# Performance work log

Measured on AMD Instinct MI355X. Metric: run time of the kernel, lower is better.

Reference implementation:

```python
import jax, jax.numpy as jnp
import numpy as np

B, C_CLS, D_WORD, J = 1024, 80, 300, 8000
IMG_CH = 2048

def setup_inputs() -> dict:
    key = jax.random.key(0)
    ks = jax.random.split(key, 9)
    return {
        'feature': jax.random.normal(ks[0], (B, IMG_CH), jnp.float32),
        'inp': jax.random.normal(ks[1], (1, C_CLS, D_WORD), jnp.float32),
        'A': jax.random.uniform(ks[2], (C_CLS, C_CLS), jnp.float32),
        'W_gc1': jax.random.normal(ks[3], (D_WORD, 1024), jnp.float32) * (1.0 / np.sqrt(1024)),
        'W_gc2': jax.random.normal(ks[4], (1024, 2048), jnp.float32) * (1.0 / np.sqrt(2048)),
        'W_img': jax.random.normal(ks[5], (J, IMG_CH), jnp.float32) * 0.02,
        'b_img': jax.random.normal(ks[6], (J,), jnp.float32) * 0.02,
        'W_cls': jax.random.normal(ks[7], (J, 2048), jnp.float32) * 0.02,
        'b_cls': jax.random.normal(ks[8], (J,), jnp.float32) * 0.02,
    }

def _gen_adj(A):
    # torch: D = A.sum(1)**-0.5; adj = (A @ diag(D)).T @ diag(D) = D[:,None]*A.T*D[None,:]
    D = jnp.power(jnp.sum(A, axis=1), -0.5)
    return D[:, None] * A.T * D[None, :]

def reference(feature, inp, A, W_gc1, W_gc2, W_img, b_img, W_cls, b_cls):
    inp0 = inp[0]                                   # [C, 300]
    adj = jax.lax.stop_gradient(_gen_adj(A))        # [C, C], .detach() in torch
    x = adj @ (inp0 @ W_gc1)                        # gc1: [C, 1024]
    x = jax.nn.leaky_relu(x, negative_slope=0.2)
    x = adj @ (x @ W_gc2)                           # gc2: [C, 2048]
    # MFB bilinear pooling (is_usemfb=True, is_hash=False -> out_in_tmp=1, eval-mode dropout=identity)
    # original: out[b,c] = sum_j (Linear_img(feature[b])[j] * Linear_cls(x_col_c)[j])
    img_proj = feature @ W_img.T + b_img            # [B, J]
    cls_proj = x @ W_cls.T + b_cls                  # [C, J]
    x_out = img_proj @ cls_proj.T                   # [B, C]
    return x_out
```

## Files before the change

### kernel.cpp

```cpp
#include <hip/hip_runtime.h>
#include <hip/hip_bf16.h>


typedef __bf16 bf16_t;
typedef __bf16 bf16x8 __attribute__((ext_vector_type(8)));
typedef float f32x4 __attribute__((ext_vector_type(4)));

#define MFMA16(a, b, c) __builtin_amdgcn_mfma_f32_16x16x32_bf16((a), (b), (c), 0, 0, 0)

#define GLOAD_LDS16(g, l)                                     \
  __builtin_amdgcn_global_load_lds(                           \
      (const __attribute__((address_space(1))) void*)(g),     \
      (__attribute__((address_space(3))) void*)(l), 16, 0, 0)

#define PIN()                                   \
  do {                                          \
    asm volatile("" ::: "memory");              \
    __builtin_amdgcn_sched_barrier(0);          \
  } while (0)

__device__ inline bf16x8 cvt8(float4 a, float4 b) {
  bf16x8 v;
  v[0] = (bf16_t)a.x; v[1] = (bf16_t)a.y; v[2] = (bf16_t)a.z; v[3] = (bf16_t)a.w;
  v[4] = (bf16_t)b.x; v[5] = (bf16_t)b.y; v[6] = (bf16_t)b.z; v[7] = (bf16_t)b.w;
  return v;
}

__global__ void k_adj(const float* __restrict__ A, float* __restrict__ adj) {
  __shared__ float Dv[80];
  int tid = threadIdx.x;
  if (tid < 80) {
    float s = 0.f;
    #pragma unroll 4
    for (int j = 0; j < 80; ++j) s += A[tid * 80 + j];
    Dv[tid] = rsqrtf(s);
  }
  __syncthreads();
  for (int idx = tid; idx < 6400; idx += blockDim.x) {
    int i = idx / 80, j = idx % 80;
    adj[idx] = Dv[i] * Dv[j] * A[j * 80 + i];
  }
}

__global__ void k_cvt0(const float* __restrict__ inp0, bf16_t* __restrict__ x0b) {
  int idx = blockIdx.x * blockDim.x + threadIdx.x;
  if (idx < 30720) {
    int c = idx / 384, k = idx % 384;
    x0b[idx] = (k < 300) ? (bf16_t)inp0[c * 300 + k] : (bf16_t)0.f;
  }
}

__global__ __launch_bounds__(256, 2) void k_gc1m(
    const bf16_t* __restrict__ x0b, const float* __restrict__ Wgc1,
    float* __restrict__ t1) {
  int tid = threadIdx.x;
  int w = tid >> 6, l = tid & 63;
  int ln = l & 15, q = l >> 4;
  int n0 = (blockIdx.x & 63) * 16;
  int kc = blockIdx.x >> 6;
  int kq = kc * 128 + w * 32 + q * 8;

  __shared__ float red[4][80][16];
  f32x4 acc[5] = {};
  bf16x8 bfrag;
  #pragma unroll
  for (int jj = 0; jj < 8; ++jj) {
    int k = kq + jj;
    int kcl = k < 300 ? k : 299;
    float wv = Wgc1[kcl * 1024 + n0 + ln];
    bfrag[jj] = (bf16_t)(k < 300 ? wv : 0.f);
  }
  #pragma unroll
  for (int mt = 0; mt < 5; ++mt) {
    bf16x8 afrag = *(const bf16x8*)(x0b + (size_t)(mt * 16 + ln) * 384 + kq);
    acc[mt] = MFMA16(afrag, bfrag, acc[mt]);
  }
  #pragma unroll
  for (int mt = 0; mt < 5; ++mt)
    #pragma unroll
    for (int reg = 0; reg < 4; ++reg)
      red[w][mt * 16 + q * 4 + reg][ln] = acc[mt][reg];
  __syncthreads();
  for (int o = tid; o < 1280; o += 256) {
    int c = o >> 4, nn = o & 15;
    atomicAdd(&t1[c * 1024 + n0 + nn],
              red[0][c][nn] + red[1][c][nn] + red[2][c][nn] + red[3][c][nn]);
  }
}

__global__ void k_adjmul_leaky(const float* __restrict__ adj, const float* __restrict__ t1,
                               bf16_t* __restrict__ x1b) {
  int idx = blockIdx.x * blockDim.x + threadIdx.x;
  int c = idx >> 10, n = idx & 1023;
  const float* ar = adj + c * 80;
  float acc = 0.f;
  #pragma unroll 4
  for (int cc = 0; cc < 80; ++cc) acc += ar[cc] * t1[cc * 1024 + n];
  x1b[idx] = (bf16_t)(acc > 0.f ? acc : 0.2f * acc);
}

__global__ __launch_bounds__(256, 2) void k_gc2m(
    const bf16_t* __restrict__ x1b, const float* __restrict__ Wgc2,
    float* __restrict__ t2) {
  int tid = threadIdx.x;
  int w = tid >> 6, l = tid & 63;
  int ln = l & 15, q = l >> 4;
  int nc = blockIdx.x & 31, kc = blockIdx.x >> 5;

  __shared__ float BsF[2 * 2048];
  auto stage = [&](int b, int k0) {
    #pragma unroll
    for (int it = 0; it < 2; ++it) {
      int slot = tid + it * 256;
      int kr = slot >> 4, nq = slot & 15;
      const float* src = Wgc2 + (size_t)(k0 + kr) * 2048 + nc * 64 + nq * 4;
      float* dst = BsF + b * 2048 + slot * 4;
      GLOAD_LDS16(src, dst);
    }
  };

  int kb = kc * 64;
  bf16x8 a0[5], a1[5];
  #pragma unroll
  for (int mt = 0; mt < 5; ++mt)
    a0[mt] = *(const bf16x8*)(x1b + (size_t)(mt * 16 + ln) * 1024 + kb + q * 8);
  PIN();
  stage(0, kb);
  PIN();
  stage(1, kb + 32);
  PIN();
  #pragma unroll
  for (int mt = 0; mt < 5; ++mt)
    a1[mt] = *(const bf16x8*)(x1b + (size_t)(mt * 16 + ln) * 1024 + kb + 32 + q * 8);
  PIN();

  f32x4 acc[5] = {};
  asm volatile("s_waitcnt vmcnt(7)" ::: "memory");
  PIN();
  __builtin_amdgcn_s_barrier();
  PIN();
  {
    bf16x8 bfrag;
    #pragma unroll
    for (int jj = 0; jj < 8; ++jj) bfrag[jj] = (bf16_t)BsF[(q * 8 + jj) * 64 + w * 16 + ln];
    #pragma unroll
    for (int mt = 0; mt < 5; ++mt) acc[mt] = MFMA16(a0[mt], bfrag, acc[mt]);
  }
  asm volatile("s_waitcnt vmcnt(5)" ::: "memory");
  PIN();
  __builtin_amdgcn_s_barrier();
  PIN();
  {
    bf16x8 bfrag;
    #pragma unroll
    for (int jj = 0; jj < 8; ++jj)
      bfrag[jj] = (bf16_t)BsF[2048 + (q * 8 + jj) * 64 + w * 16 + ln];
    #pragma unroll
    for (int mt = 0; mt < 5; ++mt) acc[mt] = MFMA16(a1[mt], bfrag, acc[mt]);
  }

  #pragma unroll
  for (int mt = 0; mt < 5; ++mt)
    #pragma unroll
    for (int reg = 0; reg < 4; ++reg)
      atomicAdd(&t2[(size_t)(mt * 16 + q * 4 + reg) * 2048 + nc * 64 + w * 16 + ln],
                acc[mt][reg]);
}

__global__ void k_adjmul_bf16(const float* __restrict__ adj, const float* __restrict__ t2,
                              bf16_t* __restrict__ x2) {
  int idx = blockIdx.x * blockDim.x + threadIdx.x;
  int c = idx >> 11, n = idx & 2047;
  const float* ar = adj + c * 80;
  float acc = 0.f;
  #pragma unroll 4
  for (int cc = 0; cc < 80; ++cc) acc += ar[cc] * t2[cc * 2048 + n];
  x2[idx] = (bf16_t)acc;
}

__global__ __launch_bounds__(256, 2) void k_clsproj(
    const float* __restrict__ Wcls, const float* __restrict__ bcls,
    const float* __restrict__ bimg, const bf16_t* __restrict__ x2,
    bf16_t* __restrict__ P, float* __restrict__ r) {
  int tid = threadIdx.x;
  int w = tid >> 6, l = tid & 63;
  int ln = l & 15, q = l >> 4;
  int j0 = blockIdx.x * 16;
  size_t jrow = (size_t)(j0 + ln) * 2048;

  __shared__ float red[4][80][16];
  __shared__ float rloc[80];
  if (tid < 80) rloc[tid] = 0.f;

  f32x4 acc[5] = {};
  int kbase = w * 512 + q * 8;

  float4 bA[2], bB[2];
  bf16x8 aF[2][5];
  {
    const float4* bp = (const float4*)(Wcls + jrow + kbase);
    bA[0] = bp[0]; bB[0] = bp[1];
    #pragma unroll
    for (int mt = 0; mt < 5; ++mt)
      aF[0][mt] = *(const bf16x8*)(x2 + (size_t)(mt * 16 + ln) * 2048 + kbase);
  }
  #pragma unroll
  for (int ks = 0; ks < 16; ++ks) {
    int cur = ks & 1, nxt = cur ^ 1;
    if (ks < 15) {
      int kq = kbase + (ks + 1) * 32;
      const float4* bp = (const float4*)(Wcls + jrow + kq);
      bA[nxt] = bp[0]; bB[nxt] = bp[1];
      #pragma unroll
      for (int mt = 0; mt < 5; ++mt)
        aF[nxt][mt] = *(const bf16x8*)(x2 + (size_t)(mt * 16 + ln) * 2048 + kq);
    }
    bf16x8 bfrag = cvt8(bA[cur], bB[cur]);
    #pragma unroll
    for (int mt = 0; mt < 5; ++mt) acc[mt] = MFMA16(aF[cur][mt], bfrag, acc[mt]);
  }
  #pragma unroll
  for (int mt = 0; mt < 5; ++mt)
    #pragma unroll
    for (int reg = 0; reg < 4; ++reg)
      red[w][mt * 16 + q * 4 + reg][ln] = acc[mt][reg];
  __syncthreads();

  for (int o = tid; o < 1280; o += 256) {
    int c = o >> 4, jj = o & 15;
    float v = red[0][c][jj] + red[1][c][jj] + red[2][c][jj] + red[3][c][jj] + bcls[j0 + jj];
    P[(size_t)c * 8000 + j0 + jj] = (bf16_t)v;
    atomicAdd(&rloc[c], bimg[j0 + jj] * v);
  }
  __syncthreads();
  if (tid < 80) atomicAdd(&r[tid], rloc[tid]);
}

__global__ __launch_bounds__(256, 2) void k_hmat(
    const float* __restrict__ Wimg, const bf16_t* __restrict__ P, float* __restrict__ H) {
  int tid = threadIdx.x;
  int w = tid >> 6, l = tid & 63;
  int ln = l & 15, q = l >> 4;
  int jc = blockIdx.x >> 4, ncg = blockIdx.x & 15;
  int jbase = jc * 160;
  int n0 = (ncg * 4 + w) * 32;

  __shared__ float Bs[4 * 3 * 1024];
  float* Bw = Bs + w * 3072;

  auto stage = [&](int buf, int jt) {
    #pragma unroll
    for (int it = 0; it < 4; ++it) {
      int row = it * 8 + (l >> 3);
      const float* src = Wimg + (size_t)(jt + row) * 2048 + n0 + (l & 7) * 4;
      float* dst = Bw + buf * 1024 + it * 256 + l * 4;
      GLOAD_LDS16(src, dst);
    }
  };
  auto loadA = [&](bf16x8* a, int jt) {
    #pragma unroll
    for (int mt = 0; mt < 5; ++mt)
      a[mt] = *(const bf16x8*)(P + (size_t)(mt * 16 + ln) * 8000 + jt + q * 8);
  };

  f32x4 acc[5][2] = {};
  bf16x8 aF[2][5];

  loadA(aF[0], jbase);
  PIN();
  stage(0, jbase);
  PIN();
  stage(1, jbase + 32);
  PIN();

  #pragma unroll
  for (int s = 0; s < 5; ++s) {
    if (s < 4) {
      loadA(aF[(s + 1) & 1], jbase + (s + 1) * 32);
      PIN();
    }
    if (s < 3) {
      stage((s + 2) % 3, jbase + (s + 2) * 32);
      PIN();
    }
    if (s < 3)       asm volatile("s_waitcnt vmcnt(13)" ::: "memory");
    else if (s == 3) asm volatile("s_waitcnt vmcnt(9)"  ::: "memory");
    else             asm volatile("s_waitcnt vmcnt(5)"  ::: "memory");
    PIN();
    const float* Bc = Bw + (s % 3) * 1024;
    bf16x8 bfrag[2];
    #pragma unroll
    for (int nt = 0; nt < 2; ++nt)
      #pragma unroll
      for (int jj = 0; jj < 8; ++jj)
        bfrag[nt][jj] = (bf16_t)Bc[(q * 8 + jj) * 32 + nt * 16 + ln];
    #pragma unroll
    for (int mt = 0; mt < 5; ++mt)
      #pragma unroll
      for (int nt = 0; nt < 2; ++nt)
        acc[mt][nt] = MFMA16(aF[s & 1][mt], bfrag[nt], acc[mt][nt]);
    PIN();
  }

  #pragma unroll
  for (int mt = 0; mt < 5; ++mt)
    #pragma unroll
    for (int nt = 0; nt < 2; ++nt)
      #pragma unroll
      for (int reg = 0; reg < 4; ++reg)
        atomicAdd(&H[(size_t)(mt * 16 + q * 4 + reg) * 2048 + n0 + nt * 16 + ln],
                  acc[mt][nt][reg]);
}

__global__ __launch_bounds__(256, 2) void k_out(
    const float* __restrict__ feat, const float* __restrict__ H,
    const float* __restrict__ r, float* __restrict__ out) {
  int tid = threadIdx.x;
  int w = tid >> 6, l = tid & 63;
  int ln = l & 15, q = l >> 4;
  int mg = blockIdx.x & 15, kc = blockIdx.x >> 4;
  int m0 = mg * 64 + w * 16;
  size_t frow = (size_t)(m0 + ln) * 2048;

  f32x4 acc[5] = {};
  int kbase = kc * 64 + q * 8;
  #pragma unroll
  for (int ks = 0; ks < 2; ++ks) {
    int kq = kbase + ks * 32;
    const float4* ap = (const float4*)(feat + frow + kq);
    bf16x8 afrag = cvt8(ap[0], ap[1]);
    #pragma unroll
    for (int nt = 0; nt < 5; ++nt) {
      const float4* hp = (const float4*)(H + (size_t)(nt * 16 + ln) * 2048 + kq);
      bf16x8 bfrag = cvt8(hp[0], hp[1]);
      acc[nt] = MFMA16(afrag, bfrag, acc[nt]);
    }
  }
  #pragma unroll
  for (int nt = 0; nt < 5; ++nt)
    #pragma unroll
    for (int reg = 0; reg < 4; ++reg) {
      int b = m0 + q * 4 + reg;
      int c = nt * 16 + ln;
      float v = acc[nt][reg];
      if (kc == 0) v += r[c];
      atomicAdd(&out[b * 80 + c], v);
    }
}

extern "C" void kernel_launch(void* const* d_in, const int* in_sizes, int n_in,
                              void* d_out, int out_size, void* d_ws, size_t ws_size,
                              hipStream_t stream) {
  const float* feature = (const float*)d_in[0];
  const float* inp     = (const float*)d_in[1];
  const float* A       = (const float*)d_in[2];
  const float* Wgc1    = (const float*)d_in[3];
  const float* Wgc2    = (const float*)d_in[4];
  const float* Wimg    = (const float*)d_in[5];
  const float* bimg    = (const float*)d_in[6];
  const float* Wcls    = (const float*)d_in[7];
  const float* bcls    = (const float*)d_in[8];
  float* out = (float*)d_out;

  char* ws = (char*)d_ws;
  float*  adj = (float*)(ws + 0);
  float*  t1  = (float*)(ws + 25600);
  bf16_t* x1b = (bf16_t*)(ws + 353280);
  float*  t2  = (float*)(ws + 517120);
  bf16_t* x2  = (bf16_t*)(ws + 1172480);
  bf16_t* P   = (bf16_t*)(ws + 1500160);
  float*  H   = (float*)(ws + 2780160);
  float*  r   = (float*)(ws + 3435520);
  bf16_t* x0b = (bf16_t*)(ws + 3435840);

  hipMemsetAsync(t1, 0, 80 * 1024 * 4, stream);
  hipMemsetAsync(t2, 0, 80 * 2048 * 4, stream);
  hipMemsetAsync(H, 0, 80 * 2048 * 4, stream);
  hipMemsetAsync(r, 0, 80 * 4, stream);
  hipMemsetAsync(out, 0, 1024 * 80 * 4, stream);

  k_adj<<<1, 128, 0, stream>>>(A, adj);
  k_cvt0<<<120, 256, 0, stream>>>(inp, x0b);
  k_gc1m<<<192, 256, 0, stream>>>(x0b, Wgc1, t1);
  k_adjmul_leaky<<<320, 256, 0, stream>>>(adj, t1, x1b);
  k_gc2m<<<512, 256, 0, stream>>>(x1b, Wgc2, t2);
  k_adjmul_bf16<<<640, 256, 0, stream>>>(adj, t2, x2);
  k_clsproj<<<500, 256, 0, stream>>>(Wcls, bcls, bimg, x2, P, r);
  k_hmat<<<800, 256, 0, stream>>>(Wimg, P, H);
  k_out<<<512, 256, 0, stream>>>(feature, H, r, out);
}
```

Baseline: 287.1 us.

## Replace LDS staging with register-pipelined direct loads across GEMM kernels, split r-vector

```diff
diff --git a/kernel.cpp b/kernel.cpp
--- a/kernel.cpp
+++ b/kernel.cpp
@@ -7,17 +7,14 @@
 typedef float f32x4 __attribute__((ext_vector_type(4)));
 
 #define MFMA16(a, b, c) __builtin_amdgcn_mfma_f32_16x16x32_bf16((a), (b), (c), 0, 0, 0)
-
-#define GLOAD_LDS16(g, l)                                     \
-  __builtin_amdgcn_global_load_lds(                           \
-      (const __attribute__((address_space(1))) void*)(g),     \
-      (__attribute__((address_space(3))) void*)(l), 16, 0, 0)
 
 #define PIN()                                   \
   do {                                          \
     asm volatile("" ::: "memory");              \
     __builtin_amdgcn_sched_barrier(0);          \
   } while (0)
+
+#define WAITV(n) asm volatile("s_waitcnt vmcnt(" #n ")" ::: "memory")
 
 __device__ inline bf16x8 cvt8(float4 a, float4 b) {
   bf16x8 v;
@@ -105,65 +102,50 @@
   int tid = threadIdx.x;
   int w = tid >> 6, l = tid & 63;
   int ln = l & 15, q = l >> 4;
-  int nc = blockIdx.x & 31, kc = blockIdx.x >> 5;
-
-  __shared__ float BsF[2 * 2048];
-  auto stage = [&](int b, int k0) {
-    #pragma unroll
-    for (int it = 0; it < 2; ++it) {
-      int slot = tid + it * 256;
-      int kr = slot >> 4, nq = slot & 15;
-      const float* src = Wgc2 + (size_t)(k0 + kr) * 2048 + nc * 64 + nq * 4;
-      float* dst = BsF + b * 2048 + slot * 4;
-      GLOAD_LDS16(src, dst);
-    }
-  };
-
-  int kb = kc * 64;
-  bf16x8 a0[5], a1[5];
+  int ng = blockIdx.x & 31, kc = blockIdx.x >> 5;
+  int n0 = ng * 64 + w * 16;
+  int k0 = kc * 128;
+
+  const bf16_t* pA[5];
   #pragma unroll
   for (int mt = 0; mt < 5; ++mt)
-    a0[mt] = *(const bf16x8*)(x1b + (size_t)(mt * 16 + ln) * 1024 + kb + q * 8);
-  PIN();
-  stage(0, kb);
-  PIN();
-  stage(1, kb + 32);
-  PIN();
+    pA[mt] = x1b + (size_t)(mt * 16 + ln) * 1024 + k0 + q * 8;
+  const float* pB = Wgc2 + (size_t)(k0 + q * 8) * 2048 + n0 + ln;
+
+  bf16x8 ar[4][5];
+  float bdw[4][8];
+  f32x4 acc[5] = {};
+
+  #pragma unroll
+  for (int s = 0; s < 4; ++s) {
+    #pragma unroll
+    for (int mt = 0; mt < 5; ++mt) ar[s][mt] = *(const bf16x8*)(pA[mt] + s * 32);
+    PIN();
+  }
+  #pragma unroll
+  for (int s = 0; s < 4; ++s) {
+    #pragma unroll
+    for (int jj = 0; jj < 8; ++jj) bdw[s][jj] = pB[(size_t)(s * 32 + jj) * 2048];
+    PIN();
+  }
+
+  #pragma unroll
+  for (int s = 0; s < 4; ++s) {
+    if (s == 0) WAITV(24); else if (s == 1) WAITV(16);
+    else if (s == 2) WAITV(8); else WAITV(0);
+    bf16x8 bfrag;
+    #pragma unroll
+    for (int jj = 0; jj < 8; ++jj) bfrag[jj] = (bf16_t)bdw[s][jj];
+    #pragma unroll
+    for (int mt = 0; mt < 5; ++mt) acc[mt] = MFMA16(ar[s][mt], bfrag, acc[mt]);
+    PIN();
+  }
+
   #pragma unroll
   for (int mt = 0; mt < 5; ++mt)
-    a1[mt] = *(const bf16x8*)(x1b + (size_t)(mt * 16 + ln) * 1024 + kb + 32 + q * 8);
-  PIN();
-
-  f32x4 acc[5] = {};
-  asm volatile("s_waitcnt vmcnt(7)" ::: "memory");
-  PIN();
-  __builtin_amdgcn_s_barrier();
-  PIN();
-  {
-    bf16x8 bfrag;
-    #pragma unroll
-    for (int jj = 0; jj < 8; ++jj) bfrag[jj] = (bf16_t)BsF[(q * 8 + jj) * 64 + w * 16 + ln];
-    #pragma unroll
-    for (int mt = 0; mt < 5; ++mt) acc[mt] = MFMA16(a0[mt], bfrag, acc[mt]);
-  }
-  asm volatile("s_waitcnt vmcnt(5)" ::: "memory");
-  PIN();
-  __builtin_amdgcn_s_barrier();
-  PIN();
-  {
-    bf16x8 bfrag;
-    #pragma unroll
-    for (int jj = 0; jj < 8; ++jj)
-      bfrag[jj] = (bf16_t)BsF[2048 + (q * 8 + jj) * 64 + w * 16 + ln];
-    #pragma unroll
-    for (int mt = 0; mt < 5; ++mt) acc[mt] = MFMA16(a1[mt], bfrag, acc[mt]);
-  }
-
-  #pragma unroll
-  for (int mt = 0; mt < 5; ++mt)
     #pragma unroll
     for (int reg = 0; reg < 4; ++reg)
-      atomicAdd(&t2[(size_t)(mt * 16 + q * 4 + reg) * 2048 + nc * 64 + w * 16 + ln],
+      atomicAdd(&t2[(size_t)(mt * 16 + q * 4 + reg) * 2048 + n0 + ln],
                 acc[mt][reg]);
 }
 
@@ -178,62 +160,99 @@
   x2[idx] = (bf16_t)acc;
 }
 
-__global__ __launch_bounds__(256, 2) void k_clsproj(
+__global__ __launch_bounds__(128, 2) void k_clsproj(
     const float* __restrict__ Wcls, const float* __restrict__ bcls,
-    const float* __restrict__ bimg, const bf16_t* __restrict__ x2,
-    bf16_t* __restrict__ P, float* __restrict__ r) {
+    const bf16_t* __restrict__ x2, bf16_t* __restrict__ P) {
   int tid = threadIdx.x;
   int w = tid >> 6, l = tid & 63;
   int ln = l & 15, q = l >> 4;
-  int j0 = blockIdx.x * 16;
-  size_t jrow = (size_t)(j0 + ln) * 2048;
-
-  __shared__ float red[4][80][16];
-  __shared__ float rloc[80];
-  if (tid < 80) rloc[tid] = 0.f;
-
+  int j0w = blockIdx.x * 32 + w * 16;
+
+  __shared__ float sm[2][16][84];
+
+  const float* pA = Wcls + (size_t)(j0w + ln) * 2048 + q * 8;
+  const bf16_t* pB[5];
+  #pragma unroll
+  for (int ct = 0; ct < 5; ++ct)
+    pB[ct] = x2 + (size_t)(ct * 16 + ln) * 2048 + q * 8;
+
+  float4 ar[8][2];
+  bf16x8 br[4][5];
   f32x4 acc[5] = {};
-  int kbase = w * 512 + q * 8;
-
-  float4 bA[2], bB[2];
-  bf16x8 aF[2][5];
-  {
-    const float4* bp = (const float4*)(Wcls + jrow + kbase);
-    bA[0] = bp[0]; bB[0] = bp[1];
-    #pragma unroll
-    for (int mt = 0; mt < 5; ++mt)
-      aF[0][mt] = *(const bf16x8*)(x2 + (size_t)(mt * 16 + ln) * 2048 + kbase);
-  }
-  #pragma unroll
-  for (int ks = 0; ks < 16; ++ks) {
-    int cur = ks & 1, nxt = cur ^ 1;
-    if (ks < 15) {
-      int kq = kbase + (ks + 1) * 32;
-      const float4* bp = (const float4*)(Wcls + jrow + kq);
-      bA[nxt] = bp[0]; bB[nxt] = bp[1];
+
+  #pragma unroll
+  for (int s = 0; s < 4; ++s) {
+    ar[s][0] = *(const float4*)(pA + s * 32);
+    ar[s][1] = *(const float4*)(pA + s * 32 + 4);
+    PIN();
+  }
+  #pragma unroll
+  for (int s = 0; s < 2; ++s) {
+    #pragma unroll
+    for (int ct = 0; ct < 5; ++ct) br[s][ct] = *(const bf16x8*)(pB[ct] + s * 32);
+    PIN();
+  }
+
+  #pragma unroll
+  for (int i = 0; i < 64; ++i) {
+    if (i <= 59) {
+      ar[(i + 4) & 7][0] = *(const float4*)(pA + (i + 4) * 32);
+      ar[(i + 4) & 7][1] = *(const float4*)(pA + (i + 4) * 32 + 4);
+      PIN();
+    }
+    if (i <= 61) {
       #pragma unroll
-      for (int mt = 0; mt < 5; ++mt)
-        aF[nxt][mt] = *(const bf16x8*)(x2 + (size_t)(mt * 16 + ln) * 2048 + kq);
-    }
-    bf16x8 bfrag = cvt8(bA[cur], bB[cur]);
-    #pragma unroll
-    for (int mt = 0; mt < 5; ++mt) acc[mt] = MFMA16(aF[cur][mt], bfrag, acc[mt]);
-  }
-  #pragma unroll
-  for (int mt = 0; mt < 5; ++mt)
+      for (int ct = 0; ct < 5; ++ct)
+        br[(i + 2) & 3][ct] = *(const bf16x8*)(pB[ct] + (i + 2) * 32);
+      PIN();
+    }
+    if (i == 0) WAITV(12);
+    else if (i < 60) WAITV(14);
+    else if (i == 60) WAITV(12);
+    else if (i == 61) WAITV(10);
+    else if (i == 62) WAITV(5);
+    else WAITV(0);
+    bf16x8 af = cvt8(ar[i & 7][0], ar[i & 7][1]);
+    #pragma unroll
+    for (int ct = 0; ct < 5; ++ct) acc[ct] = MFMA16(af, br[i & 3][ct], acc[ct]);
+    PIN();
+  }
+
+  #pragma unroll
+  for (int ct = 0; ct < 5; ++ct)
     #pragma unroll
     for (int reg = 0; reg < 4; ++reg)
-      red[w][mt * 16 + q * 4 + reg][ln] = acc[mt][reg];
+      sm[w][q * 4 + reg][ct * 16 + ln] = acc[ct][reg];
+  PIN();
+  asm volatile("s_waitcnt lgkmcnt(0)" ::: "memory");
+  PIN();
+  for (int o = l; o < 1280; o += 64) {
+    int c = o >> 4, jj = o & 15;
+    float v = sm[w][jj][c] + bcls[j0w + jj];
+    P[(size_t)c * 8000 + j0w + jj] = (bf16_t)v;
+  }
+}
+
+__global__ __launch_bounds__(256) void k_rvec(
+    const bf16_t* __restrict__ P, const float* __restrict__ bimg,
+    float* __restrict__ r) {
+  int c = blockIdx.x;
+  int tid = threadIdx.x;
+  float partial = 0.f;
+  for (int ch = tid; ch < 1000; ch += 256) {
+    bf16x8 p = *(const bf16x8*)(P + (size_t)c * 8000 + ch * 8);
+    const float4* b = (const float4*)(bimg + ch * 8);
+    float4 b0 = b[0], b1 = b[1];
+    partial += (float)p[0] * b0.x + (float)p[1] * b0.y + (float)p[2] * b0.z +
+               (float)p[3] * b0.w + (float)p[4] * b1.x + (float)p[5] * b1.y +
+               (float)p[6] * b1.z + (float)p[7] * b1.w;
+  }
+  __shared__ float red[4];
+  #pragma unroll
+  for (int off = 32; off; off >>= 1) partial += __shfl_down(partial, off);
+  if ((tid & 63) == 0) red[tid >> 6] = partial;
   __syncthreads();
-
-  for (int o = tid; o < 1280; o += 256) {
-    int c = o >> 4, jj = o & 15;
-    float v = red[0][c][jj] + red[1][c][jj] + red[2][c][jj] + red[3][c][jj] + bcls[j0 + jj];
-    P[(size_t)c * 8000 + j0 + jj] = (bf16_t)v;
-    atomicAdd(&rloc[c], bimg[j0 + jj] * v);
-  }
-  __syncthreads();
-  if (tid < 80) atomicAdd(&r[tid], rloc[tid]);
+  if (tid == 0) r[c] = red[0] + red[1] + red[2] + red[3];
 }
 
 __global__ __launch_bounds__(256, 2) void k_hmat(
@@ -241,64 +260,65 @@
   int tid = threadIdx.x;
   int w = tid >> 6, l = tid & 63;
   int ln = l & 15, q = l >> 4;
-  int jc = blockIdx.x >> 4, ncg = blockIdx.x & 15;
-  int jbase = jc * 160;
-  int n0 = (ncg * 4 + w) * 32;
-
-  __shared__ float Bs[4 * 3 * 1024];
-  float* Bw = Bs + w * 3072;
-
-  auto stage = [&](int buf, int jt) {
-    #pragma unroll
-    for (int it = 0; it < 4; ++it) {
-      int row = it * 8 + (l >> 3);
-      const float* src = Wimg + (size_t)(jt + row) * 2048 + n0 + (l & 7) * 4;
-      float* dst = Bw + buf * 1024 + it * 256 + l * 4;
-      GLOAD_LDS16(src, dst);
-    }
-  };
-  auto loadA = [&](bf16x8* a, int jt) {
-    #pragma unroll
-    for (int mt = 0; mt < 5; ++mt)
-      a[mt] = *(const bf16x8*)(P + (size_t)(mt * 16 + ln) * 8000 + jt + q * 8);
-  };
-
+  int jc = blockIdx.x >> 4, ng = blockIdx.x & 15;
+  int jbase = jc * 320;
+  int n0 = ng * 128 + w * 32;
+
+  const bf16_t* pA[5];
+  #pragma unroll
+  for (int mt = 0; mt < 5; ++mt)
+    pA[mt] = P + (size_t)(mt * 16 + ln) * 8000 + jbase + q * 8;
+  const float* pB = Wimg + (size_t)(jbase + q * 8) * 2048 + n0 + ln;
+
+  bf16x8 arr[4][5];
+  float bdw[4][16];
   f32x4 acc[5][2] = {};
-  bf16x8 aF[2][5];
-
-  loadA(aF[0], jbase);
-  PIN();
-  stage(0, jbase);
-  PIN();
-  stage(1, jbase + 32);
-  PIN();
-
-  #pragma unroll
-  for (int s = 0; s < 5; ++s) {
-    if (s < 4) {
-      loadA(aF[(s + 1) & 1], jbase + (s + 1) * 32);
-      PIN();
-    }
-    if (s < 3) {
-      stage((s + 2) % 3, jbase + (s + 2) * 32);
-      PIN();
-    }
-    if (s < 3)       asm volatile("s_waitcnt vmcnt(13)" ::: "memory");
-    else if (s == 3) asm volatile("s_waitcnt vmcnt(9)"  ::: "memory");
-    else             asm volatile("s_waitcnt vmcnt(5)"  ::: "memory");
-    PIN();
-    const float* Bc = Bw + (s % 3) * 1024;
-    bf16x8 bfrag[2];
+
+  #pragma unroll
+  for (int s = 0; s < 2; ++s) {
+    #pragma unroll
+    for (int mt = 0; mt < 5; ++mt) arr[s][mt] = *(const bf16x8*)(pA[mt] + s * 32);
+    PIN();
+  }
+  #pragma unroll
+  for (int s = 0; s < 2; ++s) {
     #pragma unroll
     for (int nt = 0; nt < 2; ++nt)
       #pragma unroll
       for (int jj = 0; jj < 8; ++jj)
-        bfrag[nt][jj] = (bf16_t)Bc[(q * 8 + jj) * 32 + nt * 16 + ln];
-    #pragma unroll
-    for (int mt = 0; mt < 5; ++mt)
+        bdw[s][nt * 8 + jj] = pB[(size_t)(s * 32 + jj) * 2048 + nt * 16];
+    PIN();
+  }
+
+  #pragma unroll
+  for (int i = 0; i < 10; ++i) {
+    if (i <= 7) {
+      #pragma unroll
+      for (int mt = 0; mt < 5; ++mt)
+        arr[(i + 2) & 3][mt] = *(const bf16x8*)(pA[mt] + (i + 2) * 32);
+      PIN();
       #pragma unroll
       for (int nt = 0; nt < 2; ++nt)
-        acc[mt][nt] = MFMA16(aF[s & 1][mt], bfrag[nt], acc[mt][nt]);
+        #pragma unroll
+        for (int jj = 0; jj < 8; ++jj)
+          bdw[(i + 2) & 3][nt * 8 + jj] = pB[(size_t)((i + 2) * 32 + jj) * 2048 + nt * 16];
+      PIN();
+    }
+    if (i == 0) WAITV(37);
+    else if (i < 8) WAITV(42);
+    else if (i == 8) WAITV(21);
+    else WAITV(0);
+    bf16x8 bf0, bf1;
+    #pragma unroll
+    for (int jj = 0; jj < 8; ++jj) {
+      bf0[jj] = (bf16_t)bdw[i & 3][jj];
+      bf1[jj] = (bf16_t)bdw[i & 3][8 + jj];
+    }
+    #pragma unroll
+    for (int mt = 0; mt < 5; ++mt) {
+      acc[mt][0] = MFMA16(arr[i & 3][mt], bf0, acc[mt][0]);
+      acc[mt][1] = MFMA16(arr[i & 3][mt], bf1, acc[mt][1]);
+    }
     PIN();
   }
 
@@ -320,22 +340,42 @@
   int ln = l & 15, q = l >> 4;
   int mg = blockIdx.x & 15, kc = blockIdx.x >> 4;
   int m0 = mg * 64 + w * 16;
-  size_t frow = (size_t)(m0 + ln) * 2048;
-
+  int kbase = kc * 64 + q * 8;
+  const float* pA = feat + (size_t)(m0 + ln) * 2048 + kbase;
+  const float* pH = H + (size_t)ln * 2048 + kbase;
+
+  float4 aw[2][2];
+  float4 bw[2][5][2];
   f32x4 acc[5] = {};
-  int kbase = kc * 64 + q * 8;
-  #pragma unroll
-  for (int ks = 0; ks < 2; ++ks) {
-    int kq = kbase + ks * 32;
-    const float4* ap = (const float4*)(feat + frow + kq);
-    bf16x8 afrag = cvt8(ap[0], ap[1]);
+
+  #pragma unroll
+  for (int s = 0; s < 2; ++s) {
+    aw[s][0] = *(const float4*)(pA + s * 32);
+    aw[s][1] = *(const float4*)(pA + s * 32 + 4);
+    PIN();
+  }
+  #pragma unroll
+  for (int s = 0; s < 2; ++s) {
     #pragma unroll
     for (int nt = 0; nt < 5; ++nt) {
-      const float4* hp = (const float4*)(H + (size_t)(nt * 16 + ln) * 2048 + kq);
-      bf16x8 bfrag = cvt8(hp[0], hp[1]);
+      bw[s][nt][0] = *(const float4*)(pH + (size_t)nt * 16 * 2048 + s * 32);
+      bw[s][nt][1] = *(const float4*)(pH + (size_t)nt * 16 * 2048 + s * 32 + 4);
+    }
+    PIN();
+  }
+
+  #pragma unroll
+  for (int s = 0; s < 2; ++s) {
+    if (s == 0) WAITV(10); else WAITV(0);
+    bf16x8 afrag = cvt8(aw[s][0], aw[s][1]);
+    #pragma unroll
+    for (int nt = 0; nt < 5; ++nt) {
+      bf16x8 bfrag = cvt8(bw[s][nt][0], bw[s][nt][1]);
       acc[nt] = MFMA16(afrag, bfrag, acc[nt]);
     }
-  }
+    PIN();
+  }
+
   #pragma unroll
   for (int nt = 0; nt < 5; ++nt)
     #pragma unroll
@@ -376,16 +416,16 @@
   hipMemsetAsync(t1, 0, 80 * 1024 * 4, stream);
   hipMemsetAsync(t2, 0, 80 * 2048 * 4, stream);
   hipMemsetAsync(H, 0, 80 * 2048 * 4, stream);
-  hipMemsetAsync(r, 0, 80 * 4, stream);
   hipMemsetAsync(out, 0, 1024 * 80 * 4, stream);
 
   k_adj<<<1, 128, 0, stream>>>(A, adj);
   k_cvt0<<<120, 256, 0, stream>>>(inp, x0b);
   k_gc1m<<<192, 256, 0, stream>>>(x0b, Wgc1, t1);
   k_adjmul_leaky<<<320, 256, 0, stream>>>(adj, t1, x1b);
-  k_gc2m<<<512, 256, 0, stream>>>(x1b, Wgc2, t2);
+  k_gc2m<<<256, 256, 0, stream>>>(x1b, Wgc2, t2);
   k_adjmul_bf16<<<640, 256, 0, stream>>>(adj, t2, x2);
-  k_clsproj<<<500, 256, 0, stream>>>(Wcls, bcls, bimg, x2, P, r);
-  k_hmat<<<800, 256, 0, stream>>>(Wimg, P, H);
+  k_clsproj<<<250, 128, 0, stream>>>(Wcls, bcls, x2, P);
+  k_rvec<<<80, 256, 0, stream>>>(P, bimg, r);
+  k_hmat<<<400, 256, 0, stream>>>(Wimg, P, H);
   k_out<<<512, 256, 0, stream>>>(feature, H, r, out);
 }
```

Measured after the change: 285.0 us. Within noise of the previous version (-0.7%).
